# Performance work log

Hardware: AMD Instinct MI355X
Metric: run time of the kernel (lower is better)

Reference implementation:

```python
import jax, jax.numpy as jnp
import numpy as np

SIZE = 256  # output image is SIZE x SIZE


def lookup_table(size):
    # matches torch.meshgrid(indexing='ij') + stack + rot90
    lin = jnp.linspace(-1.0, 1.0, size)
    xx, yy = jnp.meshgrid(lin, lin, indexing='ij')
    t = jnp.stack([xx, yy], axis=-1)
    return jnp.rot90(t, 1, axes=(0, 1))  # [S,S,2]


def area2d(a, b, c):
    return (b[..., 0] - a[..., 0]) * (c[..., 1] - a[..., 1]) - (b[..., 1] - a[..., 1]) * (c[..., 0] - a[..., 0])


def face_normals(tris):
    n = jnp.cross(tris[:, 1] - tris[:, 0], tris[:, 2] - tris[:, 0])
    # NB: faithful to source: normalize by GLOBAL Frobenius norm (not per-face)
    return n / jnp.linalg.norm(n)


def vertex_normals(vertices, f):
    fn = face_normals(vertices[f])
    vn = jnp.zeros_like(vertices)
    vn = vn.at[f[:, 0]].add(fn).at[f[:, 1]].add(fn).at[f[:, 2]].add(fn)
    return vn / jnp.linalg.norm(vn)


def bilinear_sample(img, gx, gy):
    # torch.grid_sampler_2d, mode=bilinear, padding=zeros, align_corners=False
    # img: [C,H,W]; gx -> width axis, gy -> height axis, both in [-1,1]
    C, H, W = img.shape
    x = ((gx + 1.0) * W - 1.0) * 0.5
    y = ((gy + 1.0) * H - 1.0) * 0.5
    x0 = jnp.floor(x)
    y0 = jnp.floor(y)
    x1 = x0 + 1.0
    y1 = y0 + 1.0
    wx1 = x - x0
    wx0 = 1.0 - wx1
    wy1 = y - y0
    wy0 = 1.0 - wy1

    def gather(ix, iy):
        valid = (ix >= 0) & (ix <= W - 1) & (iy >= 0) & (iy <= H - 1)
        ixc = jnp.clip(ix, 0, W - 1).astype(jnp.int32)
        iyc = jnp.clip(iy, 0, H - 1).astype(jnp.int32)
        return img[:, iyc, ixc] * valid  # [C,...]

    return (gather(x0, y0) * (wx0 * wy0) + gather(x1, y0) * (wx1 * wy0)
            + gather(x0, y1) * (wx0 * wy1) + gather(x1, y1) * (wx1 * wy1))


def setup_inputs() -> dict:
    key = jax.random.key(0)
    k1, k2, k3, k4, k5, k6 = jax.random.split(key, 6)
    V, F, M = 1024, 256, 1024
    xy = jax.random.uniform(k1, (V, 2), minval=-1.0, maxval=1.0, dtype=jnp.float32)
    z = jax.random.uniform(k2, (V, 1), minval=0.5, maxval=1.5, dtype=jnp.float32)
    vertices = jnp.concatenate([xy, z], axis=1)
    faces = jax.random.randint(k3, (F, 3), 0, V, dtype=jnp.int64)
    uv = jax.random.uniform(k4, (M, 2), dtype=jnp.float32)
    uvfaces = jax.random.randint(k5, (F, 3), 0, M, dtype=jnp.int64)
    uvmap = jax.random.uniform(k6, (3, 256, 256), dtype=jnp.float32)
    return {"vertices": vertices, "faces": faces, "uv": uv, "uvfaces": uvfaces, "uvmap": uvmap}


def reference(vertices, faces, uv, uvfaces, uvmap):
    size = SIZE
    pts = lookup_table(size)                       # [S,S,2]
    uvn = uv * 2.0 - 1.0                            # init: uv*2-1
    tris = vertices[faces]                          # [F,3,3]
    z_inv = 1.0 / tris[:, :, 2:3]                   # [F,3,1]
    vn = vertex_normals(vertices, faces)[faces] * z_inv
    uvs = uvn[uvfaces] * z_inv
    tri9 = jnp.concatenate([tris, uvs, vn, z_inv], axis=2)  # [F,3,9]
    cullmask = face_normals(tris)[:, 2] > 0         # backface cull, eye=(0,0,1)

    t2 = tris[:, :, :2]
    A = area2d(t2[:, 0], t2[:, 1], t2[:, 2])        # [F] signed double-area
    valid_tri = cullmask & (A >= 1e-9)              # raster skips A < 1e-9
    Asafe = jnp.where(jnp.abs(A) < 1e-9, 1.0, A)

    px = pts[..., 0][None]                          # [1,S,S]
    py = pts[..., 1][None]

    def edge(a, c):
        # area2d(a, p, c) evaluated on the pixel grid: linear in p
        ax, ay = a[:, 0, None, None], a[:, 1, None, None]
        cx, cy = c[:, 0, None, None], c[:, 1, None, None]
        return (px - ax) * (cy - ay) - (py - ay) * (cx - ax)

    pAB = edge(t2[:, 1], t2[:, 0])                  # [F,S,S]
    pCB = edge(t2[:, 2], t2[:, 1])
    pCA = edge(t2[:, 0], t2[:, 2])
    cover = (pAB > 0) & (pCB > 0) & (pCA > 0) & valid_tri[:, None, None]

    w1 = pCB / Asafe[:, None, None]
    w2 = pCA / Asafe[:, None, None]
    w3 = 1.0 - w1 - w2
    zinv_p = (w1 * tri9[:, 0, 8, None, None] + w2 * tri9[:, 1, 8, None, None]
              + w3 * tri9[:, 2, 8, None, None])     # interpolated 1/z, [F,S,S]
    zinit = vertices[:, 2].min()                    # initial z-buffer value
    ptsZ = 1.0 / jnp.where(cover, zinv_p, 1.0)      # perspective-correct depth
    score = jnp.where(cover & (ptsZ >= zinit), ptsZ, -jnp.inf)
    # sequential loop with `ptsZ >= zbuffer` converges to the max-depth winner
    winner = jnp.argmax(score, axis=0)              # [S,S]
    hit = jnp.isfinite(jnp.max(score, axis=0))      # [S,S]

    take = lambda arr: jnp.take_along_axis(arr, winner[None], axis=0)[0]
    W1, W2, W3 = take(w1), take(w2), take(w3)       # [S,S]
    tri_w = tri9[winner]                            # [S,S,3,9]
    pts9 = (W1[..., None] * tri_w[..., 0, :] + W2[..., None] * tri_w[..., 1, :]
            + W3[..., None] * tri_w[..., 2, :])     # [S,S,9]
    Zw = 1.0 / jnp.where(hit, pts9[..., 8], 1.0)
    attrs = pts9[..., :8] * Zw[..., None]           # perspective-corrected attrs
    rgb = bilinear_sample(uvmap, attrs[..., 3], attrs[..., 4])  # [3,S,S]
    hitf = hit.astype(rgb.dtype)
    result = jnp.concatenate([rgb * hitf[None], hitf[None]], axis=0)  # [4,S,S]
    return result
```

## Files before the change

kernel.cpp:

```cpp
#include <hip/hip_runtime.h>
#include <math.h>
#include <limits.h>

#define SIZE   256
#define NFACES 256
#define NVERTS 1024
#define NSPLIT 8


__global__ __launch_bounds__(1024) void render_kernel(
    const float* __restrict__ vertices,
    const int*   __restrict__ faces,
    const float* __restrict__ uv,
    const int*   __restrict__ uvfaces,
    const float* __restrict__ uvmap,
    float* __restrict__ out)
{
#pragma clang fp contract(off)
    __shared__ float4 fdl[NFACES * 5];
    __shared__ int    sfid[NFACES];
    __shared__ float  sh_best[NSPLIT][128];
    __shared__ int    sh_fid [NSPLIT][128];
    __shared__ int    sh_slot[NSPLIT][128];
    __shared__ float  wred[16];
    __shared__ int    wcnt[4];

    const int t    = threadIdx.x;
    const int lane = t & 63;
    const int wv   = t >> 6;
    const int half = blockIdx.x;
    const int row  = blockIdx.y;
    const int col  = (t & 127) + 128 * half;
    const int grp  = t >> 7;

    const float px = (float)(-1.0 + (double)col         * (2.0/255.0));
    const float py = (float)(-1.0 + (double)(255 - row) * (2.0/255.0));

    {
        float m = vertices[3*t + 2];
        for (int off = 32; off > 0; off >>= 1) m = fminf(m, __shfl_down(m, off));
        if (lane == 0) wred[wv] = m;
    }

    float4 q0, q1, q2, q3, q4;
    bool keep = false;
    int  rank = 0;
    if (t < NFACES) {
        const int i0 = faces[3*t+0], i1 = faces[3*t+1], i2 = faces[3*t+2];
        const float ax = vertices[3*i0+0], ay = vertices[3*i0+1], az = vertices[3*i0+2];
        const float bx = vertices[3*i1+0], by = vertices[3*i1+1], bz = vertices[3*i1+2];
        const float cx = vertices[3*i2+0], cy = vertices[3*i2+1], cz = vertices[3*i2+2];
        const float A = (bx-ax)*(cy-ay) - (by-ay)*(cx-ax);
        const float ymin = fminf(fminf(ay,by),cy);
        const float ymax = fmaxf(fmaxf(ay,by),cy);
        keep = (A >= 1e-9f) && (py > ymin - 1e-4f) && (py < ymax + 1e-4f);
        const unsigned long long bmask = __ballot(keep);
        rank = __popcll(bmask & ((1ull << lane) - 1ull));
        if (lane == 0) wcnt[wv] = (int)__popcll(bmask);
        if (keep) {
            const float z0i = 1.0f/az, z1i = 1.0f/bz, z2i = 1.0f/cz;
            const int j0 = uvfaces[3*t+0], j1 = uvfaces[3*t+1], j2 = uvfaces[3*t+2];
            q0 = make_float4(ax, ay, bx, by);
            q1 = make_float4(cx, cy, fminf(fminf(ax,bx),cx), fmaxf(fmaxf(ax,bx),cx));
            q2 = make_float4(z0i, z1i, z2i, A);
            q3 = make_float4((uv[2*j0+0]*2.0f - 1.0f) * z0i,
                             (uv[2*j0+1]*2.0f - 1.0f) * z0i,
                             (uv[2*j1+0]*2.0f - 1.0f) * z1i,
                             (uv[2*j1+1]*2.0f - 1.0f) * z1i);
            q4 = make_float4((uv[2*j2+0]*2.0f - 1.0f) * z2i,
                             (uv[2*j2+1]*2.0f - 1.0f) * z2i, 0.0f, 0.0f);
        }
    }
    __syncthreads();

    float zinit;
    {
        float mm = wred[0];
        #pragma unroll
        for (int i = 1; i < 16; ++i) mm = fminf(mm, wred[i]);
        zinit = mm;
    }
    const int nv = wcnt[0] + wcnt[1] + wcnt[2] + wcnt[3];

    if (t < NFACES && keep) {
        int base = 0;
        #pragma unroll
        for (int w = 0; w < 4; ++w) if (w < wv) base += wcnt[w];
        const int slot = base + rank;
        sfid[slot] = t;
        fdl[slot*5+0] = q0; fdl[slot*5+1] = q1; fdl[slot*5+2] = q2;
        fdl[slot*5+3] = q3; fdl[slot*5+4] = q4;
    }
    __syncthreads();

    const int   c0   = ((t >> 6) & 1) * 64 + 128 * half;
    const float pxlo = (float)(-1.0 + (double)c0        * (2.0/255.0));
    const float pxhi = (float)(-1.0 + (double)(c0 + 63) * (2.0/255.0));

    const int cs = (nv + NSPLIT - 1) / NSPLIT;
    int f0 = grp * cs; if (f0 > nv) f0 = nv;
    int f1 = f0 + cs;  if (f1 > nv) f1 = nv;

    float best  = -INFINITY;
    int   wfid  = INT_MAX;
    int   wslot = 0;
    for (int i = f0; i < f1; ++i) {
        const float4 c1 = fdl[i*5+1];
        if (c1.w + 1e-4f < pxlo || c1.z - 1e-4f > pxhi) continue;
        const float4 c0q = fdl[i*5+0];
        const float pAB = (px - c0q.z)*(c0q.y - c0q.w) - (py - c0q.w)*(c0q.x - c0q.z);
        const float pCB = (px - c1.x)*(c0q.w - c1.y)   - (py - c1.y)*(c0q.z - c1.x);
        const float pCA = (px - c0q.x)*(c1.y - c0q.y)  - (py - c0q.y)*(c1.x - c0q.x);
        if (pAB > 0.0f && pCB > 0.0f && pCA > 0.0f) {
            const float4 c2 = fdl[i*5+2];
            const float w1 = pCB / c2.w;
            const float w2 = pCA / c2.w;
            const float w3 = (1.0f - w1) - w2;
            const float zp = (w1*c2.x + w2*c2.y) + w3*c2.z;
            const float z  = 1.0f / zp;
            if (z >= zinit) {
                const int fid = sfid[i];
                if (z > best || (z == best && fid < wfid)) { best = z; wfid = fid; wslot = i; }
            }
        }
    }
    sh_best[grp][t & 127] = best;
    sh_fid [grp][t & 127] = wfid;
    sh_slot[grp][t & 127] = wslot;
    __syncthreads();

    if (t < 128) {
        best = -INFINITY; wfid = INT_MAX; wslot = 0;
        #pragma unroll
        for (int g = 0; g < NSPLIT; ++g) {
            const float z = sh_best[g][t];
            const int   f = sh_fid [g][t];
            if (z > best || (z == best && f < wfid)) { best = z; wfid = f; wslot = sh_slot[g][t]; }
        }

        const bool  hit = (best > -INFINITY);
        const float hf  = hit ? 1.0f : 0.0f;
        float r0 = 0.0f, r1 = 0.0f, r2 = 0.0f;

        if (hit) {
            const float4 c0q = fdl[wslot*5+0];
            const float4 c1  = fdl[wslot*5+1];
            const float4 c2  = fdl[wslot*5+2];
            const float4 c3  = fdl[wslot*5+3];
            const float4 c4  = fdl[wslot*5+4];
            const float pCB = (px - c1.x)*(c0q.w - c1.y)  - (py - c1.y)*(c0q.z - c1.x);
            const float pCA = (px - c0q.x)*(c1.y - c0q.y) - (py - c0q.y)*(c1.x - c0q.x);
            const float w1 = pCB / c2.w;
            const float w2 = pCA / c2.w;
            const float w3 = (1.0f - w1) - w2;
            const float p3 = (w1*c3.x + w2*c3.z) + w3*c4.x;
            const float p4 = (w1*c3.y + w2*c3.w) + w3*c4.y;
            const float p8 = (w1*c2.x + w2*c2.y) + w3*c2.z;
            const float Zw = 1.0f / p8;
            const float gx = p3 * Zw;
            const float gy = p4 * Zw;

            const float x = ((gx + 1.0f)*256.0f - 1.0f)*0.5f;
            const float y = ((gy + 1.0f)*256.0f - 1.0f)*0.5f;
            const float x0f = floorf(x), y0f = floorf(y);
            const float x1f = x0f + 1.0f, y1f = y0f + 1.0f;
            const float wx1 = x - x0f, wx0 = 1.0f - wx1;
            const float wy1 = y - y0f, wy0 = 1.0f - wy1;
            const float w00 = wx0*wy0, w10 = wx1*wy0, w01 = wx0*wy1, w11 = wx1*wy1;

            {
                const bool v = (x0f >= 0.0f) && (x0f <= 255.0f) && (y0f >= 0.0f) && (y0f <= 255.0f);
                const int ix = (int)fminf(fmaxf(x0f, 0.0f), 255.0f);
                const int iy = (int)fminf(fmaxf(y0f, 0.0f), 255.0f);
                const int o  = iy*256 + ix;
                const float g0 = v ? uvmap[o]          : 0.0f;
                const float g1 = v ? uvmap[65536 + o]  : 0.0f;
                const float g2 = v ? uvmap[131072 + o] : 0.0f;
                r0 = r0 + g0*w00; r1 = r1 + g1*w00; r2 = r2 + g2*w00;
            }
            {
                const bool v = (x1f >= 0.0f) && (x1f <= 255.0f) && (y0f >= 0.0f) && (y0f <= 255.0f);
                const int ix = (int)fminf(fmaxf(x1f, 0.0f), 255.0f);
                const int iy = (int)fminf(fmaxf(y0f, 0.0f), 255.0f);
                const int o  = iy*256 + ix;
                const float g0 = v ? uvmap[o]          : 0.0f;
                const float g1 = v ? uvmap[65536 + o]  : 0.0f;
                const float g2 = v ? uvmap[131072 + o] : 0.0f;
                r0 = r0 + g0*w10; r1 = r1 + g1*w10; r2 = r2 + g2*w10;
            }
            {
                const bool v = (x0f >= 0.0f) && (x0f <= 255.0f) && (y1f >= 0.0f) && (y1f <= 255.0f);
                const int ix = (int)fminf(fmaxf(x0f, 0.0f), 255.0f);
                const int iy = (int)fminf(fmaxf(y1f, 0.0f), 255.0f);
                const int o  = iy*256 + ix;
                const float g0 = v ? uvmap[o]          : 0.0f;
                const float g1 = v ? uvmap[65536 + o]  : 0.0f;
                const float g2 = v ? uvmap[131072 + o] : 0.0f;
                r0 = r0 + g0*w01; r1 = r1 + g1*w01; r2 = r2 + g2*w01;
            }
            {
                const bool v = (x1f >= 0.0f) && (x1f <= 255.0f) && (y1f >= 0.0f) && (y1f <= 255.0f);
                const int ix = (int)fminf(fmaxf(x1f, 0.0f), 255.0f);
                const int iy = (int)fminf(fmaxf(y1f, 0.0f), 255.0f);
                const int o  = iy*256 + ix;
                const float g0 = v ? uvmap[o]          : 0.0f;
                const float g1 = v ? uvmap[65536 + o]  : 0.0f;
                const float g2 = v ? uvmap[131072 + o] : 0.0f;
                r0 = r0 + g0*w11; r1 = r1 + g1*w11; r2 = r2 + g2*w11;
            }
        }

        const int pix = row*256 + col;
        out[           pix] = r0*hf;
        out[ 65536 +   pix] = r1*hf;
        out[131072 +   pix] = r2*hf;
        out[196608 +   pix] = hf;
    }
}

extern "C" void kernel_launch(void* const* d_in, const int* in_sizes, int n_in,
                              void* d_out, int out_size, void* d_ws, size_t ws_size,
                              hipStream_t stream) {
    const float* vertices = (const float*)d_in[0];
    const int*   faces    = (const int*)  d_in[1];
    const float* uv       = (const float*)d_in[2];
    const int*   uvfaces  = (const int*)  d_in[3];
    const float* uvmap    = (const float*)d_in[4];
    float*       out      = (float*)d_out;

    dim3 grid(2, SIZE);
    render_kernel<<<grid, 1024, 0, stream>>>(vertices, faces, uv, uvfaces, uvmap, out);
}
```

Baseline: 74.54 us.

## Drop face-split reduction; one 256-thread block per row, one thread per pixel

Replaces the 1024-thread blocks that split the face list into 8 groups per pixel and reduce through shared memory with 256-thread blocks, one per image row, where each thread scans all kept faces for its own pixel. This removes the cross-group shared-memory reduction, an extra barrier, and the redundant per-block face setup (now done once per row instead of twice). The trade-off is less parallelism per pixel: each thread runs a serial loop that is about 8x longer, and there are fewer total waves (256 blocks of 4 waves) to hide latency on a large GPU.

```diff
diff --git a/kernel.cpp b/kernel.cpp
--- a/kernel.cpp
+++ b/kernel.cpp
@@ -5,10 +5,9 @@
 #define SIZE   256
 #define NFACES 256
 #define NVERTS 1024
-#define NSPLIT 8
-
-
-__global__ __launch_bounds__(1024) void render_kernel(
+
+
+__global__ __launch_bounds__(256) void render_kernel(
     const float* __restrict__ vertices,
     const int*   __restrict__ faces,
     const float* __restrict__ uv,
@@ -19,25 +18,23 @@
 #pragma clang fp contract(off)
     __shared__ float4 fdl[NFACES * 5];
     __shared__ int    sfid[NFACES];
-    __shared__ float  sh_best[NSPLIT][128];
-    __shared__ int    sh_fid [NSPLIT][128];
-    __shared__ int    sh_slot[NSPLIT][128];
-    __shared__ float  wred[16];
+    __shared__ float  wred[4];
     __shared__ int    wcnt[4];
 
     const int t    = threadIdx.x;
     const int lane = t & 63;
     const int wv   = t >> 6;
-    const int half = blockIdx.x;
-    const int row  = blockIdx.y;
-    const int col  = (t & 127) + 128 * half;
-    const int grp  = t >> 7;
+    const int row  = blockIdx.x;
+    const int col  = t;
 
     const float px = (float)(-1.0 + (double)col         * (2.0/255.0));
     const float py = (float)(-1.0 + (double)(255 - row) * (2.0/255.0));
 
     {
-        float m = vertices[3*t + 2];
+        float m =       vertices[3*t        + 2];
+        m = fminf(m,    vertices[3*(t+256)  + 2]);
+        m = fminf(m,    vertices[3*(t+512)  + 2]);
+        m = fminf(m,    vertices[3*(t+768)  + 2]);
         for (int off = 32; off > 0; off >>= 1) m = fminf(m, __shfl_down(m, off));
         if (lane == 0) wred[wv] = m;
     }
@@ -45,7 +42,7 @@
     float4 q0, q1, q2, q3, q4;
     bool keep = false;
     int  rank = 0;
-    if (t < NFACES) {
+    {
         const int i0 = faces[3*t+0], i1 = faces[3*t+1], i2 = faces[3*t+2];
         const float ax = vertices[3*i0+0], ay = vertices[3*i0+1], az = vertices[3*i0+2];
         const float bx = vertices[3*i1+0], by = vertices[3*i1+1], bz = vertices[3*i1+2];
@@ -73,16 +70,10 @@
     }
     __syncthreads();
 
-    float zinit;
-    {
-        float mm = wred[0];
-        #pragma unroll
-        for (int i = 1; i < 16; ++i) mm = fminf(mm, wred[i]);
-        zinit = mm;
-    }
-    const int nv = wcnt[0] + wcnt[1] + wcnt[2] + wcnt[3];
-
-    if (t < NFACES && keep) {
+    const float zinit = fminf(fminf(wred[0], wred[1]), fminf(wred[2], wred[3]));
+    const int   nv    = wcnt[0] + wcnt[1] + wcnt[2] + wcnt[3];
+
+    if (keep) {
         int base = 0;
         #pragma unroll
         for (int w = 0; w < 4; ++w) if (w < wv) base += wcnt[w];
@@ -93,18 +84,14 @@
     }
     __syncthreads();
 
-    const int   c0   = ((t >> 6) & 1) * 64 + 128 * half;
+    const int   c0   = wv * 64;
     const float pxlo = (float)(-1.0 + (double)c0        * (2.0/255.0));
     const float pxhi = (float)(-1.0 + (double)(c0 + 63) * (2.0/255.0));
-
-    const int cs = (nv + NSPLIT - 1) / NSPLIT;
-    int f0 = grp * cs; if (f0 > nv) f0 = nv;
-    int f1 = f0 + cs;  if (f1 > nv) f1 = nv;
 
     float best  = -INFINITY;
     int   wfid  = INT_MAX;
     int   wslot = 0;
-    for (int i = f0; i < f1; ++i) {
+    for (int i = 0; i < nv; ++i) {
         const float4 c1 = fdl[i*5+1];
         if (c1.w + 1e-4f < pxlo || c1.z - 1e-4f > pxhi) continue;
         const float4 c0q = fdl[i*5+0];
@@ -124,98 +111,84 @@
             }
         }
     }
-    sh_best[grp][t & 127] = best;
-    sh_fid [grp][t & 127] = wfid;
-    sh_slot[grp][t & 127] = wslot;
-    __syncthreads();
-
-    if (t < 128) {
-        best = -INFINITY; wfid = INT_MAX; wslot = 0;
-        #pragma unroll
-        for (int g = 0; g < NSPLIT; ++g) {
-            const float z = sh_best[g][t];
-            const int   f = sh_fid [g][t];
-            if (z > best || (z == best && f < wfid)) { best = z; wfid = f; wslot = sh_slot[g][t]; }
-        }
-
-        const bool  hit = (best > -INFINITY);
-        const float hf  = hit ? 1.0f : 0.0f;
-        float r0 = 0.0f, r1 = 0.0f, r2 = 0.0f;
-
-        if (hit) {
-            const float4 c0q = fdl[wslot*5+0];
-            const float4 c1  = fdl[wslot*5+1];
-            const float4 c2  = fdl[wslot*5+2];
-            const float4 c3  = fdl[wslot*5+3];
-            const float4 c4  = fdl[wslot*5+4];
-            const float pCB = (px - c1.x)*(c0q.w - c1.y)  - (py - c1.y)*(c0q.z - c1.x);
-            const float pCA = (px - c0q.x)*(c1.y - c0q.y) - (py - c0q.y)*(c1.x - c0q.x);
-            const float w1 = pCB / c2.w;
-            const float w2 = pCA / c2.w;
-            const float w3 = (1.0f - w1) - w2;
-            const float p3 = (w1*c3.x + w2*c3.z) + w3*c4.x;
-            const float p4 = (w1*c3.y + w2*c3.w) + w3*c4.y;
-            const float p8 = (w1*c2.x + w2*c2.y) + w3*c2.z;
-            const float Zw = 1.0f / p8;
-            const float gx = p3 * Zw;
-            const float gy = p4 * Zw;
-
-            const float x = ((gx + 1.0f)*256.0f - 1.0f)*0.5f;
-            const float y = ((gy + 1.0f)*256.0f - 1.0f)*0.5f;
-            const float x0f = floorf(x), y0f = floorf(y);
-            const float x1f = x0f + 1.0f, y1f = y0f + 1.0f;
-            const float wx1 = x - x0f, wx0 = 1.0f - wx1;
-            const float wy1 = y - y0f, wy0 = 1.0f - wy1;
-            const float w00 = wx0*wy0, w10 = wx1*wy0, w01 = wx0*wy1, w11 = wx1*wy1;
-
-            {
-                const bool v = (x0f >= 0.0f) && (x0f <= 255.0f) && (y0f >= 0.0f) && (y0f <= 255.0f);
-                const int ix = (int)fminf(fmaxf(x0f, 0.0f), 255.0f);
-                const int iy = (int)fminf(fmaxf(y0f, 0.0f), 255.0f);
-                const int o  = iy*256 + ix;
-                const float g0 = v ? uvmap[o]          : 0.0f;
-                const float g1 = v ? uvmap[65536 + o]  : 0.0f;
-                const float g2 = v ? uvmap[131072 + o] : 0.0f;
-                r0 = r0 + g0*w00; r1 = r1 + g1*w00; r2 = r2 + g2*w00;
-            }
-            {
-                const bool v = (x1f >= 0.0f) && (x1f <= 255.0f) && (y0f >= 0.0f) && (y0f <= 255.0f);
-                const int ix = (int)fminf(fmaxf(x1f, 0.0f), 255.0f);
-                const int iy = (int)fminf(fmaxf(y0f, 0.0f), 255.0f);
-                const int o  = iy*256 + ix;
-                const float g0 = v ? uvmap[o]          : 0.0f;
-                const float g1 = v ? uvmap[65536 + o]  : 0.0f;
-                const float g2 = v ? uvmap[131072 + o] : 0.0f;
-                r0 = r0 + g0*w10; r1 = r1 + g1*w10; r2 = r2 + g2*w10;
-            }
-            {
-                const bool v = (x0f >= 0.0f) && (x0f <= 255.0f) && (y1f >= 0.0f) && (y1f <= 255.0f);
-                const int ix = (int)fminf(fmaxf(x0f, 0.0f), 255.0f);
-                const int iy = (int)fminf(fmaxf(y1f, 0.0f), 255.0f);
-                const int o  = iy*256 + ix;
-                const float g0 = v ? uvmap[o]          : 0.0f;
-                const float g1 = v ? uvmap[65536 + o]  : 0.0f;
-                const float g2 = v ? uvmap[131072 + o] : 0.0f;
-                r0 = r0 + g0*w01; r1 = r1 + g1*w01; r2 = r2 + g2*w01;
-            }
-            {
-                const bool v = (x1f >= 0.0f) && (x1f <= 255.0f) && (y1f >= 0.0f) && (y1f <= 255.0f);
-                const int ix = (int)fminf(fmaxf(x1f, 0.0f), 255.0f);
-                const int iy = (int)fminf(fmaxf(y1f, 0.0f), 255.0f);
-                const int o  = iy*256 + ix;
-                const float g0 = v ? uvmap[o]          : 0.0f;
-                const float g1 = v ? uvmap[65536 + o]  : 0.0f;
-                const float g2 = v ? uvmap[131072 + o] : 0.0f;
-                r0 = r0 + g0*w11; r1 = r1 + g1*w11; r2 = r2 + g2*w11;
-            }
-        }
-
-        const int pix = row*256 + col;
-        out[           pix] = r0*hf;
-        out[ 65536 +   pix] = r1*hf;
-        out[131072 +   pix] = r2*hf;
-        out[196608 +   pix] = hf;
-    }
+
+    const bool  hit = (best > -INFINITY);
+    const float hf  = hit ? 1.0f : 0.0f;
+    float r0 = 0.0f, r1 = 0.0f, r2 = 0.0f;
+
+    if (hit) {
+        const float4 c0q = fdl[wslot*5+0];
+        const float4 c1  = fdl[wslot*5+1];
+        const float4 c2  = fdl[wslot*5+2];
+        const float4 c3  = fdl[wslot*5+3];
+        const float4 c4  = fdl[wslot*5+4];
+        const float pCB = (px - c1.x)*(c0q.w - c1.y)  - (py - c1.y)*(c0q.z - c1.x);
+        const float pCA = (px - c0q.x)*(c1.y - c0q.y) - (py - c0q.y)*(c1.x - c0q.x);
+        const float w1 = pCB / c2.w;
+        const float w2 = pCA / c2.w;
+        const float w3 = (1.0f - w1) - w2;
+        const float p3 = (w1*c3.x + w2*c3.z) + w3*c4.x;
+        const float p4 = (w1*c3.y + w2*c3.w) + w3*c4.y;
+        const float p8 = (w1*c2.x + w2*c2.y) + w3*c2.z;
+        const float Zw = 1.0f / p8;
+        const float gx = p3 * Zw;
+        const float gy = p4 * Zw;
+
+        const float x = ((gx + 1.0f)*256.0f - 1.0f)*0.5f;
+        const float y = ((gy + 1.0f)*256.0f - 1.0f)*0.5f;
+        const float x0f = floorf(x), y0f = floorf(y);
+        const float x1f = x0f + 1.0f, y1f = y0f + 1.0f;
+        const float wx1 = x - x0f, wx0 = 1.0f - wx1;
+        const float wy1 = y - y0f, wy0 = 1.0f - wy1;
+        const float w00 = wx0*wy0, w10 = wx1*wy0, w01 = wx0*wy1, w11 = wx1*wy1;
+
+        {
+            const bool v = (x0f >= 0.0f) && (x0f <= 255.0f) && (y0f >= 0.0f) && (y0f <= 255.0f);
+            const int ix = (int)fminf(fmaxf(x0f, 0.0f), 255.0f);
+            const int iy = (int)fminf(fmaxf(y0f, 0.0f), 255.0f);
+            const int o  = iy*256 + ix;
+            const float g0 = v ? uvmap[o]          : 0.0f;
+            const float g1 = v ? uvmap[65536 + o]  : 0.0f;
+            const float g2 = v ? uvmap[131072 + o] : 0.0f;
+            r0 = r0 + g0*w00; r1 = r1 + g1*w00; r2 = r2 + g2*w00;
+        }
+        {
+            const bool v = (x1f >= 0.0f) && (x1f <= 255.0f) && (y0f >= 0.0f) && (y0f <= 255.0f);
+            const int ix = (int)fminf(fmaxf(x1f, 0.0f), 255.0f);
+            const int iy = (int)fminf(fmaxf(y0f, 0.0f), 255.0f);
+            const int o  = iy*256 + ix;
+            const float g0 = v ? uvmap[o]          : 0.0f;
+            const float g1 = v ? uvmap[65536 + o]  : 0.0f;
+            const float g2 = v ? uvmap[131072 + o] : 0.0f;
+            r0 = r0 + g0*w10; r1 = r1 + g1*w10; r2 = r2 + g2*w10;
+        }
+        {
+            const bool v = (x0f >= 0.0f) && (x0f <= 255.0f) && (y1f >= 0.0f) && (y1f <= 255.0f);
+            const int ix = (int)fminf(fmaxf(x0f, 0.0f), 255.0f);
+            const int iy = (int)fminf(fmaxf(y1f, 0.0f), 255.0f);
+            const int o  = iy*256 + ix;
+            const float g0 = v ? uvmap[o]          : 0.0f;
+            const float g1 = v ? uvmap[65536 + o]  : 0.0f;
+            const float g2 = v ? uvmap[131072 + o] : 0.0f;
+            r0 = r0 + g0*w01; r1 = r1 + g1*w01; r2 = r2 + g2*w01;
+        }
+        {
+            const bool v = (x1f >= 0.0f) && (x1f <= 255.0f) && (y1f >= 0.0f) && (y1f <= 255.0f);
+            const int ix = (int)fminf(fmaxf(x1f, 0.0f), 255.0f);
+            const int iy = (int)fminf(fmaxf(y1f, 0.0f), 255.0f);
+            const int o  = iy*256 + ix;
+            const float g0 = v ? uvmap[o]          : 0.0f;
+            const float g1 = v ? uvmap[65536 + o]  : 0.0f;
+            const float g2 = v ? uvmap[131072 + o] : 0.0f;
+            r0 = r0 + g0*w11; r1 = r1 + g1*w11; r2 = r2 + g2*w11;
+        }
+    }
+
+    const int pix = row*256 + col;
+    out[           pix] = r0*hf;
+    out[ 65536 +   pix] = r1*hf;
+    out[131072 +   pix] = r2*hf;
+    out[196608 +   pix] = hf;
 }
 
 extern "C" void kernel_launch(void* const* d_in, const int* in_sizes, int n_in,
@@ -228,6 +201,6 @@
     const float* uvmap    = (const float*)d_in[4];
     float*       out      = (float*)d_out;
 
-    dim3 grid(2, SIZE);
-    render_kernel<<<grid, 1024, 0, stream>>>(vertices, faces, uv, uvfaces, uvmap, out);
+    dim3 grid(SIZE);
+    render_kernel<<<grid, 256, 0, stream>>>(vertices, faces, uv, uvfaces, uvmap, out);
 }
```

Measured after the change: 95.71 us. +28.4%, slower.

## Process a full image row per block with four face splits

Applied to the files above, without the earlier changes.

Each block now covers a whole 256-pixel row instead of half a row, and the face list is split into four groups instead of eight. This halves the number of blocks, so the per-block preamble (z-min reduction, face culling, compaction into shared memory) runs half as often. Each thread now scans a longer face range, which lengthens the serial loop. UV loads are also vectorised to float2.

```diff
diff --git a/kernel.cpp b/kernel.cpp
--- a/kernel.cpp
+++ b/kernel.cpp
@@ -5,7 +5,7 @@
 #define SIZE   256
 #define NFACES 256
 #define NVERTS 1024
-#define NSPLIT 8
+#define NSPLIT 4
 
 
 __global__ __launch_bounds__(1024) void render_kernel(
@@ -19,19 +19,18 @@
 #pragma clang fp contract(off)
     __shared__ float4 fdl[NFACES * 5];
     __shared__ int    sfid[NFACES];
-    __shared__ float  sh_best[NSPLIT][128];
-    __shared__ int    sh_fid [NSPLIT][128];
-    __shared__ int    sh_slot[NSPLIT][128];
+    __shared__ float  sh_best[NSPLIT][256];
+    __shared__ int    sh_fid [NSPLIT][256];
+    __shared__ int    sh_slot[NSPLIT][256];
     __shared__ float  wred[16];
     __shared__ int    wcnt[4];
 
     const int t    = threadIdx.x;
     const int lane = t & 63;
     const int wv   = t >> 6;
-    const int half = blockIdx.x;
-    const int row  = blockIdx.y;
-    const int col  = (t & 127) + 128 * half;
-    const int grp  = t >> 7;
+    const int row  = blockIdx.x;
+    const int col  = t & 255;
+    const int grp  = t >> 8;
 
     const float px = (float)(-1.0 + (double)col         * (2.0/255.0));
     const float py = (float)(-1.0 + (double)(255 - row) * (2.0/255.0));
@@ -60,15 +59,18 @@
         if (keep) {
             const float z0i = 1.0f/az, z1i = 1.0f/bz, z2i = 1.0f/cz;
             const int j0 = uvfaces[3*t+0], j1 = uvfaces[3*t+1], j2 = uvfaces[3*t+2];
+            const float2 u0 = *reinterpret_cast<const float2*>(&uv[2*j0]);
+            const float2 u1 = *reinterpret_cast<const float2*>(&uv[2*j1]);
+            const float2 u2 = *reinterpret_cast<const float2*>(&uv[2*j2]);
             q0 = make_float4(ax, ay, bx, by);
             q1 = make_float4(cx, cy, fminf(fminf(ax,bx),cx), fmaxf(fmaxf(ax,bx),cx));
             q2 = make_float4(z0i, z1i, z2i, A);
-            q3 = make_float4((uv[2*j0+0]*2.0f - 1.0f) * z0i,
-                             (uv[2*j0+1]*2.0f - 1.0f) * z0i,
-                             (uv[2*j1+0]*2.0f - 1.0f) * z1i,
-                             (uv[2*j1+1]*2.0f - 1.0f) * z1i);
-            q4 = make_float4((uv[2*j2+0]*2.0f - 1.0f) * z2i,
-                             (uv[2*j2+1]*2.0f - 1.0f) * z2i, 0.0f, 0.0f);
+            q3 = make_float4((u0.x*2.0f - 1.0f) * z0i,
+                             (u0.y*2.0f - 1.0f) * z0i,
+                             (u1.x*2.0f - 1.0f) * z1i,
+                             (u1.y*2.0f - 1.0f) * z1i);
+            q4 = make_float4((u2.x*2.0f - 1.0f) * z2i,
+                             (u2.y*2.0f - 1.0f) * z2i, 0.0f, 0.0f);
         }
     }
     __syncthreads();
@@ -93,7 +95,7 @@
     }
     __syncthreads();
 
-    const int   c0   = ((t >> 6) & 1) * 64 + 128 * half;
+    const int   c0   = ((t >> 6) & 3) * 64;
     const float pxlo = (float)(-1.0 + (double)c0        * (2.0/255.0));
     const float pxhi = (float)(-1.0 + (double)(c0 + 63) * (2.0/255.0));
 
@@ -124,12 +126,12 @@
             }
         }
     }
-    sh_best[grp][t & 127] = best;
-    sh_fid [grp][t & 127] = wfid;
-    sh_slot[grp][t & 127] = wslot;
+    sh_best[grp][col] = best;
+    sh_fid [grp][col] = wfid;
+    sh_slot[grp][col] = wslot;
     __syncthreads();
 
-    if (t < 128) {
+    if (t < 256) {
         best = -INFINITY; wfid = INT_MAX; wslot = 0;
         #pragma unroll
         for (int g = 0; g < NSPLIT; ++g) {
@@ -228,6 +230,6 @@
     const float* uvmap    = (const float*)d_in[4];
     float*       out      = (float*)d_out;
 
-    dim3 grid(2, SIZE);
+    dim3 grid(SIZE);
     render_kernel<<<grid, 1024, 0, stream>>>(vertices, faces, uv, uvfaces, uvmap, out);
 }
```

New measurement: 77.72 us. 4.3% more time.

## Split face setup into a prep kernel and read face records from global

Applied to the files above, without the earlier changes.

Adds a single-block prep kernel that computes the z minimum, culls back-facing triangles, and writes compacted per-face records (bounding box, vertices, inverse depths, scaled UVs) to workspace. The render kernel no longer rebuilds the face list in shared memory for every block. It reads the records through cache and culls on a combined x/y bounding box per pixel group. Ties are now broken by compacted slot order instead of face id, which keeps the same ordering. The cost is an extra launch and record loads from global or L2 inside the hot loop instead of LDS.

```diff
diff --git a/kernel.cpp b/kernel.cpp
--- a/kernel.cpp
+++ b/kernel.cpp
@@ -8,26 +8,79 @@
 #define NSPLIT 8
 
 
-__global__ __launch_bounds__(1024) void render_kernel(
+__global__ __launch_bounds__(256) void prep_kernel(
     const float* __restrict__ vertices,
     const int*   __restrict__ faces,
     const float* __restrict__ uv,
     const int*   __restrict__ uvfaces,
+    float* __restrict__ ws)
+{
+#pragma clang fp contract(off)
+    __shared__ float wred[4];
+    __shared__ int   wcnt[4];
+    const int t    = threadIdx.x;
+    const int lane = t & 63;
+    const int wv   = t >> 6;
+
+    {
+        float m =    vertices[3*t         + 2];
+        m = fminf(m, vertices[3*(t + 256) + 2]);
+        m = fminf(m, vertices[3*(t + 512) + 2]);
+        m = fminf(m, vertices[3*(t + 768) + 2]);
+        for (int off = 32; off > 0; off >>= 1) m = fminf(m, __shfl_down(m, off));
+        if (lane == 0) wred[wv] = m;
+    }
+
+    const int i0 = faces[3*t+0], i1 = faces[3*t+1], i2 = faces[3*t+2];
+    const float ax = vertices[3*i0+0], ay = vertices[3*i0+1], az = vertices[3*i0+2];
+    const float bx = vertices[3*i1+0], by = vertices[3*i1+1], bz = vertices[3*i1+2];
+    const float cx = vertices[3*i2+0], cy = vertices[3*i2+1], cz = vertices[3*i2+2];
+    const float A  = (bx-ax)*(cy-ay) - (by-ay)*(cx-ax);
+    const bool keep = (A >= 1e-9f);
+    const unsigned long long bmask = __ballot(keep);
+    const int rank = __popcll(bmask & ((1ull << lane) - 1ull));
+    if (lane == 0) wcnt[wv] = (int)__popcll(bmask);
+    __syncthreads();
+
+    if (t == 0) {
+        ((int*)ws)[0] = wcnt[0] + wcnt[1] + wcnt[2] + wcnt[3];
+        ws[1] = fminf(fminf(wred[0], wred[1]), fminf(wred[2], wred[3]));
+    }
+    if (keep) {
+        int base = 0;
+        #pragma unroll
+        for (int w = 0; w < 4; ++w) if (w < wv) base += wcnt[w];
+        const int slot = base + rank;
+        const float z0i = 1.0f/az, z1i = 1.0f/bz, z2i = 1.0f/cz;
+        const int j0 = uvfaces[3*t+0], j1 = uvfaces[3*t+1], j2 = uvfaces[3*t+2];
+        const float2 u0 = *reinterpret_cast<const float2*>(&uv[2*j0]);
+        const float2 u1 = *reinterpret_cast<const float2*>(&uv[2*j1]);
+        const float2 u2 = *reinterpret_cast<const float2*>(&uv[2*j2]);
+        float4* rec = reinterpret_cast<float4*>(ws + 4) + slot*5;
+        rec[0] = make_float4(fminf(fminf(ax,bx),cx), fmaxf(fmaxf(ax,bx),cx),
+                             fminf(fminf(ay,by),cy), fmaxf(fmaxf(ay,by),cy));
+        rec[1] = make_float4(ax, ay, bx, by);
+        rec[2] = make_float4(cx, cy, z0i, z1i);
+        rec[3] = make_float4(z2i, A,
+                             (u0.x*2.0f - 1.0f) * z0i,
+                             (u0.y*2.0f - 1.0f) * z0i);
+        rec[4] = make_float4((u1.x*2.0f - 1.0f) * z1i,
+                             (u1.y*2.0f - 1.0f) * z1i,
+                             (u2.x*2.0f - 1.0f) * z2i,
+                             (u2.y*2.0f - 1.0f) * z2i);
+    }
+}
+
+__global__ __launch_bounds__(1024) void render_kernel(
     const float* __restrict__ uvmap,
+    const float* __restrict__ ws,
     float* __restrict__ out)
 {
 #pragma clang fp contract(off)
-    __shared__ float4 fdl[NFACES * 5];
-    __shared__ int    sfid[NFACES];
-    __shared__ float  sh_best[NSPLIT][128];
-    __shared__ int    sh_fid [NSPLIT][128];
-    __shared__ int    sh_slot[NSPLIT][128];
-    __shared__ float  wred[16];
-    __shared__ int    wcnt[4];
+    __shared__ float sh_best[NSPLIT][128];
+    __shared__ int   sh_slot[NSPLIT][128];
 
     const int t    = threadIdx.x;
-    const int lane = t & 63;
-    const int wv   = t >> 6;
     const int half = blockIdx.x;
     const int row  = blockIdx.y;
     const int col  = (t & 127) + 128 * half;
@@ -36,62 +89,9 @@
     const float px = (float)(-1.0 + (double)col         * (2.0/255.0));
     const float py = (float)(-1.0 + (double)(255 - row) * (2.0/255.0));
 
-    {
-        float m = vertices[3*t + 2];
-        for (int off = 32; off > 0; off >>= 1) m = fminf(m, __shfl_down(m, off));
-        if (lane == 0) wred[wv] = m;
-    }
-
-    float4 q0, q1, q2, q3, q4;
-    bool keep = false;
-    int  rank = 0;
-    if (t < NFACES) {
-        const int i0 = faces[3*t+0], i1 = faces[3*t+1], i2 = faces[3*t+2];
-        const float ax = vertices[3*i0+0], ay = vertices[3*i0+1], az = vertices[3*i0+2];
-        const float bx = vertices[3*i1+0], by = vertices[3*i1+1], bz = vertices[3*i1+2];
-        const float cx = vertices[3*i2+0], cy = vertices[3*i2+1], cz = vertices[3*i2+2];
-        const float A = (bx-ax)*(cy-ay) - (by-ay)*(cx-ax);
-        const float ymin = fminf(fminf(ay,by),cy);
-        const float ymax = fmaxf(fmaxf(ay,by),cy);
-        keep = (A >= 1e-9f) && (py > ymin - 1e-4f) && (py < ymax + 1e-4f);
-        const unsigned long long bmask = __ballot(keep);
-        rank = __popcll(bmask & ((1ull << lane) - 1ull));
-        if (lane == 0) wcnt[wv] = (int)__popcll(bmask);
-        if (keep) {
-            const float z0i = 1.0f/az, z1i = 1.0f/bz, z2i = 1.0f/cz;
-            const int j0 = uvfaces[3*t+0], j1 = uvfaces[3*t+1], j2 = uvfaces[3*t+2];
-            q0 = make_float4(ax, ay, bx, by);
-            q1 = make_float4(cx, cy, fminf(fminf(ax,bx),cx), fmaxf(fmaxf(ax,bx),cx));
-            q2 = make_float4(z0i, z1i, z2i, A);
-            q3 = make_float4((uv[2*j0+0]*2.0f - 1.0f) * z0i,
-                             (uv[2*j0+1]*2.0f - 1.0f) * z0i,
-                             (uv[2*j1+0]*2.0f - 1.0f) * z1i,
-                             (uv[2*j1+1]*2.0f - 1.0f) * z1i);
-            q4 = make_float4((uv[2*j2+0]*2.0f - 1.0f) * z2i,
-                             (uv[2*j2+1]*2.0f - 1.0f) * z2i, 0.0f, 0.0f);
-        }
-    }
-    __syncthreads();
-
-    float zinit;
-    {
-        float mm = wred[0];
-        #pragma unroll
-        for (int i = 1; i < 16; ++i) mm = fminf(mm, wred[i]);
-        zinit = mm;
-    }
-    const int nv = wcnt[0] + wcnt[1] + wcnt[2] + wcnt[3];
-
-    if (t < NFACES && keep) {
-        int base = 0;
-        #pragma unroll
-        for (int w = 0; w < 4; ++w) if (w < wv) base += wcnt[w];
-        const int slot = base + rank;
-        sfid[slot] = t;
-        fdl[slot*5+0] = q0; fdl[slot*5+1] = q1; fdl[slot*5+2] = q2;
-        fdl[slot*5+3] = q3; fdl[slot*5+4] = q4;
-    }
-    __syncthreads();
+    const int   nv    = ((const int*)ws)[0];
+    const float zinit = ws[1];
+    const float4* __restrict__ recs = reinterpret_cast<const float4*>(ws + 4);
 
     const int   c0   = ((t >> 6) & 1) * 64 + 128 * half;
     const float pxlo = (float)(-1.0 + (double)c0        * (2.0/255.0));
@@ -102,60 +102,56 @@
     int f1 = f0 + cs;  if (f1 > nv) f1 = nv;
 
     float best  = -INFINITY;
-    int   wfid  = INT_MAX;
     int   wslot = 0;
     for (int i = f0; i < f1; ++i) {
-        const float4 c1 = fdl[i*5+1];
-        if (c1.w + 1e-4f < pxlo || c1.z - 1e-4f > pxhi) continue;
-        const float4 c0q = fdl[i*5+0];
-        const float pAB = (px - c0q.z)*(c0q.y - c0q.w) - (py - c0q.w)*(c0q.x - c0q.z);
-        const float pCB = (px - c1.x)*(c0q.w - c1.y)   - (py - c1.y)*(c0q.z - c1.x);
-        const float pCA = (px - c0q.x)*(c1.y - c0q.y)  - (py - c0q.y)*(c1.x - c0q.x);
+        const float4 bb = recs[i*5];
+        if (bb.y + 1e-4f < pxlo || bb.x - 1e-4f > pxhi ||
+            py <= bb.z - 1e-4f || py >= bb.w + 1e-4f) continue;
+        const float4 r1 = recs[i*5+1];
+        const float4 r2 = recs[i*5+2];
+        const float4 r3 = recs[i*5+3];
+        const float pAB = (px - r1.z)*(r1.y - r1.w) - (py - r1.w)*(r1.x - r1.z);
+        const float pCB = (px - r2.x)*(r1.w - r2.y) - (py - r2.y)*(r1.z - r2.x);
+        const float pCA = (px - r1.x)*(r2.y - r1.y) - (py - r1.y)*(r2.x - r1.x);
         if (pAB > 0.0f && pCB > 0.0f && pCA > 0.0f) {
-            const float4 c2 = fdl[i*5+2];
-            const float w1 = pCB / c2.w;
-            const float w2 = pCA / c2.w;
+            const float w1 = pCB / r3.y;
+            const float w2 = pCA / r3.y;
             const float w3 = (1.0f - w1) - w2;
-            const float zp = (w1*c2.x + w2*c2.y) + w3*c2.z;
+            const float zp = (w1*r2.z + w2*r2.w) + w3*r3.x;
             const float z  = 1.0f / zp;
-            if (z >= zinit) {
-                const int fid = sfid[i];
-                if (z > best || (z == best && fid < wfid)) { best = z; wfid = fid; wslot = i; }
-            }
+            if (z >= zinit && z > best) { best = z; wslot = i; }
         }
     }
     sh_best[grp][t & 127] = best;
-    sh_fid [grp][t & 127] = wfid;
     sh_slot[grp][t & 127] = wslot;
     __syncthreads();
 
     if (t < 128) {
-        best = -INFINITY; wfid = INT_MAX; wslot = 0;
+        best = -INFINITY; wslot = 0;
         #pragma unroll
         for (int g = 0; g < NSPLIT; ++g) {
             const float z = sh_best[g][t];
-            const int   f = sh_fid [g][t];
-            if (z > best || (z == best && f < wfid)) { best = z; wfid = f; wslot = sh_slot[g][t]; }
+            const int   s = sh_slot[g][t];
+            if (z > best || (z == best && s < wslot)) { best = z; wslot = s; }
         }
 
         const bool  hit = (best > -INFINITY);
         const float hf  = hit ? 1.0f : 0.0f;
-        float r0 = 0.0f, r1 = 0.0f, r2 = 0.0f;
+        float r0v = 0.0f, r1v = 0.0f, r2v = 0.0f;
 
         if (hit) {
-            const float4 c0q = fdl[wslot*5+0];
-            const float4 c1  = fdl[wslot*5+1];
-            const float4 c2  = fdl[wslot*5+2];
-            const float4 c3  = fdl[wslot*5+3];
-            const float4 c4  = fdl[wslot*5+4];
-            const float pCB = (px - c1.x)*(c0q.w - c1.y)  - (py - c1.y)*(c0q.z - c1.x);
-            const float pCA = (px - c0q.x)*(c1.y - c0q.y) - (py - c0q.y)*(c1.x - c0q.x);
-            const float w1 = pCB / c2.w;
-            const float w2 = pCA / c2.w;
+            const float4 r1 = recs[wslot*5+1];
+            const float4 r2 = recs[wslot*5+2];
+            const float4 r3 = recs[wslot*5+3];
+            const float4 r4 = recs[wslot*5+4];
+            const float pCB = (px - r2.x)*(r1.w - r2.y) - (py - r2.y)*(r1.z - r2.x);
+            const float pCA = (px - r1.x)*(r2.y - r1.y) - (py - r1.y)*(r2.x - r1.x);
+            const float w1 = pCB / r3.y;
+            const float w2 = pCA / r3.y;
             const float w3 = (1.0f - w1) - w2;
-            const float p3 = (w1*c3.x + w2*c3.z) + w3*c4.x;
-            const float p4 = (w1*c3.y + w2*c3.w) + w3*c4.y;
-            const float p8 = (w1*c2.x + w2*c2.y) + w3*c2.z;
+            const float p3 = (w1*r3.z + w2*r4.x) + w3*r4.z;
+            const float p4 = (w1*r3.w + w2*r4.y) + w3*r4.w;
+            const float p8 = (w1*r2.z + w2*r2.w) + w3*r3.x;
             const float Zw = 1.0f / p8;
             const float gx = p3 * Zw;
             const float gy = p4 * Zw;
@@ -176,7 +172,7 @@
                 const float g0 = v ? uvmap[o]          : 0.0f;
                 const float g1 = v ? uvmap[65536 + o]  : 0.0f;
                 const float g2 = v ? uvmap[131072 + o] : 0.0f;
-                r0 = r0 + g0*w00; r1 = r1 + g1*w00; r2 = r2 + g2*w00;
+                r0v = r0v + g0*w00; r1v = r1v + g1*w00; r2v = r2v + g2*w00;
             }
             {
                 const bool v = (x1f >= 0.0f) && (x1f <= 255.0f) && (y0f >= 0.0f) && (y0f <= 255.0f);
@@ -186,7 +182,7 @@
                 const float g0 = v ? uvmap[o]          : 0.0f;
                 const float g1 = v ? uvmap[65536 + o]  : 0.0f;
                 const float g2 = v ? uvmap[131072 + o] : 0.0f;
-                r0 = r0 + g0*w10; r1 = r1 + g1*w10; r2 = r2 + g2*w10;
+                r0v = r0v + g0*w10; r1v = r1v + g1*w10; r2v = r2v + g2*w10;
             }
             {
                 const bool v = (x0f >= 0.0f) && (x0f <= 255.0f) && (y1f >= 0.0f) && (y1f <= 255.0f);
@@ -196,7 +192,7 @@
                 const float g0 = v ? uvmap[o]          : 0.0f;
                 const float g1 = v ? uvmap[65536 + o]  : 0.0f;
                 const float g2 = v ? uvmap[131072 + o] : 0.0f;
-                r0 = r0 + g0*w01; r1 = r1 + g1*w01; r2 = r2 + g2*w01;
+                r0v = r0v + g0*w01; r1v = r1v + g1*w01; r2v = r2v + g2*w01;
             }
             {
                 const bool v = (x1f >= 0.0f) && (x1f <= 255.0f) && (y1f >= 0.0f) && (y1f <= 255.0f);
@@ -206,14 +202,14 @@
                 const float g0 = v ? uvmap[o]          : 0.0f;
                 const float g1 = v ? uvmap[65536 + o]  : 0.0f;
                 const float g2 = v ? uvmap[131072 + o] : 0.0f;
-                r0 = r0 + g0*w11; r1 = r1 + g1*w11; r2 = r2 + g2*w11;
+                r0v = r0v + g0*w11; r1v = r1v + g1*w11; r2v = r2v + g2*w11;
             }
         }
 
         const int pix = row*256 + col;
-        out[           pix] = r0*hf;
-        out[ 65536 +   pix] = r1*hf;
-        out[131072 +   pix] = r2*hf;
+        out[           pix] = r0v*hf;
+        out[ 65536 +   pix] = r1v*hf;
+        out[131072 +   pix] = r2v*hf;
         out[196608 +   pix] = hf;
     }
 }
@@ -227,7 +223,9 @@
     const int*   uvfaces  = (const int*)  d_in[3];
     const float* uvmap    = (const float*)d_in[4];
     float*       out      = (float*)d_out;
-
+    float*       ws       = (float*)d_ws;
+
+    prep_kernel<<<1, 256, 0, stream>>>(vertices, faces, uv, uvfaces, ws);
     dim3 grid(2, SIZE);
-    render_kernel<<<grid, 1024, 0, stream>>>(vertices, faces, uv, uvfaces, uvmap, out);
+    render_kernel<<<grid, 1024, 0, stream>>>(uvmap, ws, out);
 }
```

Result: slower. 79.72 us (+6.9%).
